# Kernel optimization log

Measured on AMD Instinct MI355X. Metric: run time of the kernel, lower is better.

Reference implementation:

```python
import jax, jax.numpy as jnp
import numpy as np

S, B, D = 2048, 2, 4096
H, KVH, HD = 32, 8, 128          # n_heads_q, n_kv_heads, head_dim
NREP = H // KVH                  # GQA repeat factor
ROPE_BASE = 10000.0


def _rope(x, cos, sin):
    # x: [B, S, h, HD]; cos/sin: [S, HD//2]
    xr = x.reshape(x.shape[:-1] + (-1, 2))
    x0, x1 = xr[..., 0], xr[..., 1]
    c = cos[None, :, None, :]
    s = sin[None, :, None, :]
    out = jnp.stack([x0 * c - x1 * s, x0 * s + x1 * c], axis=-1)
    return out.reshape(x.shape)


def setup_inputs() -> dict:
    key = jax.random.key(0)
    k0, k1, k2, k3, k4 = jax.random.split(key, 5)
    x = jax.random.normal(k0, (S, B, D), jnp.float32)
    inv_freq = 1.0 / (ROPE_BASE ** (np.arange(0, HD, 2, dtype=np.float64) / HD))  # [HD//2]
    t = np.arange(S, dtype=np.float64)[:, None] * inv_freq[None, :]               # [S, HD//2]
    freqs_cos = jnp.asarray(np.cos(t), jnp.float32)
    freqs_sin = jnp.asarray(np.sin(t), jnp.float32)
    scale = 0.02
    wq = jax.random.normal(k1, (H * HD, D), jnp.float32) * scale
    wk = jax.random.normal(k2, (KVH * HD, D), jnp.float32) * scale
    wv = jax.random.normal(k3, (KVH * HD, D), jnp.float32) * scale
    wo = jax.random.normal(k4, (D, H * HD), jnp.float32) * scale
    return {"x": x, "start_pos": 0, "freqs_cos": freqs_cos, "freqs_sin": freqs_sin,
            "wq": wq, "wk": wk, "wv": wv, "wo": wo}


def reference(x, start_pos, freqs_cos, freqs_sin, wq, wk, wv, wo):
    seq_len, batch, _ = x.shape
    # QKV projections (torch Linear: y = x @ W^T), then [S,B,*] -> [B,S,h,HD]
    q = (x @ wq.T).transpose(1, 0, 2).reshape(batch, seq_len, H, HD)
    k = (x @ wk.T).transpose(1, 0, 2).reshape(batch, seq_len, KVH, HD)
    v = (x @ wv.T).transpose(1, 0, 2).reshape(batch, seq_len, KVH, HD)
    # RoPE on q and k
    q = _rope(q, freqs_cos, freqs_sin)
    k = _rope(k, freqs_cos, freqs_sin)
    # repeat_kv (GQA)
    k = jnp.repeat(k, NREP, axis=2)
    v = jnp.repeat(v, NREP, axis=2)
    # [B, H, S, HD]
    q = q.transpose(0, 2, 1, 3)
    k = k.transpose(0, 2, 1, 3)
    v = v.transpose(0, 2, 1, 3)
    # causal scaled dot-product attention (SDPA is_causal=True equivalent)
    scores = jnp.einsum('bhqd,bhkd->bhqk', q, k) / np.float32(np.sqrt(HD))
    causal = jnp.tril(jnp.ones((seq_len, seq_len), dtype=bool))
    scores = jnp.where(causal[None, None], scores, jnp.float32(-jnp.inf))
    probs = jax.nn.softmax(scores.astype(jnp.float32), axis=-1).astype(q.dtype)
    out = jnp.einsum('bhqk,bhkd->bhqd', probs, v)
    # [B,H,S,HD] -> [B,S,H*HD] -> [S,B,H*HD]
    out = out.transpose(0, 2, 1, 3).reshape(batch, seq_len, H * HD).transpose(1, 0, 2)
    return out @ wo.T
```

## Files before the change

### kernel.cpp

```cpp
#include <hip/hip_runtime.h>

typedef __attribute__((ext_vector_type(8))) short s16x8;
typedef __attribute__((ext_vector_type(8))) __bf16 bf16x8;
typedef __attribute__((ext_vector_type(4))) float f32x4;

#define S_LEN 2048
#define KDIM  4096
#define CSOFT 0.12751743f

__device__ __forceinline__ unsigned short f2bf(float f) {
  unsigned u = __builtin_bit_cast(unsigned, f);
  u += 0x7fffu + ((u >> 16) & 1u);
  return (unsigned short)(u >> 16);
}

__device__ __forceinline__ f32x4 mfma_bf16(s16x8 a, s16x8 b, f32x4 c) {
  return __builtin_amdgcn_mfma_f32_16x16x32_bf16(
      __builtin_bit_cast(bf16x8, a), __builtin_bit_cast(bf16x8, b), c, 0, 0, 0);
}

__device__ __forceinline__ void gload_lds16(const unsigned short* g, void* l) {
  __builtin_amdgcn_global_load_lds(
      (const __attribute__((address_space(1))) void*)g,
      (__attribute__((address_space(3))) void*)l, 16, 0, 0);
}

__global__ void cvt_bf16(const float* __restrict__ in,
                         unsigned short* __restrict__ out, int n8) {
  int i = blockIdx.x * 256 + threadIdx.x;
  if (i >= n8) return;
  const float* p = in + (size_t)i * 8;
  f32x4 a = *(const f32x4*)(p);
  f32x4 b = *(const f32x4*)(p + 4);
  s16x8 v;
  v[0] = (short)f2bf(a[0]); v[1] = (short)f2bf(a[1]);
  v[2] = (short)f2bf(a[2]); v[3] = (short)f2bf(a[3]);
  v[4] = (short)f2bf(b[0]); v[5] = (short)f2bf(b[1]);
  v[6] = (short)f2bf(b[2]); v[7] = (short)f2bf(b[3]);
  *(s16x8*)(out + (size_t)i * 8) = v;
}

template <int EPI>
__global__ __launch_bounds__(512, 1)
void gemm256(const unsigned short* __restrict__ A,
             const unsigned short* __restrict__ B,
             void* __restrict__ Out,
             const float* __restrict__ cosT,
             const float* __restrict__ sinT) {
  const int K = KDIM;
  __shared__ __align__(16) unsigned short As[2 * 2 * 8192];
  __shared__ __align__(16) unsigned short Bs[2 * 2 * 8192];

  const int tid = threadIdx.x;
  const int lane = tid & 63, wid = tid >> 6;
  const int l15 = lane & 15, l4 = lane >> 4;
  const int wr = wid >> 2, wc = wid & 3;

  int bid = blockIdx.x;
  int wg = (bid & 7) * 32 + (bid >> 3);
  const int rt = wg >> 4, ct = wg & 15;
  const int row0 = rt * 256, col0 = ct * 256;

  const int ch0 = tid, ch1 = 512 + tid;
  const int sr0 = ch0 >> 3, u0 = (ch0 & 7) ^ (sr0 & 7);
  const int sr1 = ch1 >> 3, u1 = (ch1 & 7) ^ (sr1 & 7);
  const unsigned short* A0p = A + (size_t)(row0 + sr0) * K + u0 * 8;
  const unsigned short* A1p = A + (size_t)(row0 + sr1) * K + u1 * 8;
  const unsigned short* B0p = B + (size_t)(col0 + sr0) * K + u0 * 8;
  const unsigned short* B1p = B + (size_t)(col0 + sr1) * K + u1 * 8;

  const int rdo0 = l15 * 128 + ((l4 ^ (l15 & 7)) << 4);
  const int rdo1 = l15 * 128 + (((4 | l4) ^ (l15 & 7)) << 4);

  f32x4 acc[8][4];
#pragma unroll
  for (int m = 0; m < 8; m++)
#pragma unroll
    for (int n = 0; n < 4; n++) acc[m][n] = f32x4{0.f, 0.f, 0.f, 0.f};

  auto stageA = [&](int buf, int h, int kt) {
    char* d = (char*)As + buf * 32768 + h * 16384 + wid * 1024;
    size_t so = (size_t)h * 128 * K + kt;
    gload_lds16(A0p + so, d);
    gload_lds16(A1p + so, d + 8192);
  };
  auto stageB = [&](int buf, int h, int kt) {
    char* d = (char*)Bs + buf * 32768 + h * 16384 + wid * 1024;
    size_t so = (size_t)h * 128 * K + kt;
    gload_lds16(B0p + so, d);
    gload_lds16(B1p + so, d + 8192);
  };
  auto bar = [&]() {
    __builtin_amdgcn_s_barrier();
    __builtin_amdgcn_sched_barrier(0);
  };
  auto quad = [&](const s16x8* ak0, const s16x8* ak1,
                  const s16x8* bk0, const s16x8* bk1, int mb, int nb) {
    __builtin_amdgcn_s_setprio(1);
#pragma unroll
    for (int mi = 0; mi < 4; mi++)
#pragma unroll
      for (int ni = 0; ni < 2; ni++) {
        acc[mb + mi][nb + ni] =
            mfma_bf16(ak0[mi], bk0[ni], acc[mb + mi][nb + ni]);
        acc[mb + mi][nb + ni] =
            mfma_bf16(ak1[mi], bk1[ni], acc[mb + mi][nb + ni]);
      }
    __builtin_amdgcn_s_setprio(0);
  };

  auto tile4 = [&](int buf, auto st1, auto st2, auto st3, auto st4,
                   int vmEnd) {
    const char* Ab = (const char*)As + buf * 32768 + wr * 16384;
    const char* Bb = (const char*)Bs + buf * 32768 + (wc >> 1) * 16384 +
                     (wc & 1) * 8192;
    s16x8 a0k0[4], a0k1[4], a1k0[4], a1k1[4];
    s16x8 b0k0[2], b0k1[2], b1k0[2], b1k1[2];

#pragma unroll
    for (int mi = 0; mi < 4; mi++) {
      a0k0[mi] = *(const s16x8*)(Ab + mi * 2048 + rdo0);
      a0k1[mi] = *(const s16x8*)(Ab + mi * 2048 + rdo1);
    }
#pragma unroll
    for (int ni = 0; ni < 2; ni++) {
      b0k0[ni] = *(const s16x8*)(Bb + ni * 2048 + rdo0);
      b0k1[ni] = *(const s16x8*)(Bb + ni * 2048 + rdo1);
    }
    st1();
    bar();
    quad(a0k0, a0k1, b0k0, b0k1, 0, 0);
    bar();

#pragma unroll
    for (int mi = 0; mi < 4; mi++) {
      a1k0[mi] = *(const s16x8*)(Ab + 8192 + mi * 2048 + rdo0);
      a1k1[mi] = *(const s16x8*)(Ab + 8192 + mi * 2048 + rdo1);
    }
#pragma unroll
    for (int ni = 0; ni < 2; ni++) {
      b1k0[ni] = *(const s16x8*)(Bb + 4096 + ni * 2048 + rdo0);
      b1k1[ni] = *(const s16x8*)(Bb + 4096 + ni * 2048 + rdo1);
    }
    st2();
    bar();
    quad(a1k0, a1k1, b0k0, b0k1, 4, 0);
    bar();

    st3();
    bar();
    quad(a0k0, a0k1, b1k0, b1k1, 0, 2);
    bar();

    st4();
    bar();
    quad(a1k0, a1k1, b1k0, b1k1, 4, 2);
    if (vmEnd == 4) {
      asm volatile("s_waitcnt vmcnt(4)" ::: "memory");
    } else if (vmEnd == 0) {
      asm volatile("s_waitcnt vmcnt(0)" ::: "memory");
    }
    bar();
  };
  auto nop = [&]() {};

  stageA(0, 0, 0);
  stageA(0, 1, 0);
  stageB(0, 0, 0);
  stageB(0, 1, 0);
  stageA(1, 0, 64);
  stageA(1, 1, 64);
  asm volatile("s_waitcnt vmcnt(4)" ::: "memory");
  bar();

  for (int j = 0; j < 31; j++) {
    const int k1 = (2 * j + 1) * 64, k2 = (2 * j + 2) * 64,
              k3 = (2 * j + 3) * 64;
    tile4(0, [&] { stageB(1, 0, k1); }, [&] { stageB(1, 1, k1); },
          [&] { stageA(0, 0, k2); }, [&] { stageA(0, 1, k2); }, 4);
    tile4(1, [&] { stageB(0, 0, k2); }, [&] { stageB(0, 1, k2); },
          [&] { stageA(1, 0, k3); }, [&] { stageA(1, 1, k3); }, 4);
  }
  {
    const int k1 = 63 * 64;
    tile4(0, [&] { stageB(1, 0, k1); }, [&] { stageB(1, 1, k1); }, nop, nop,
          0);
    tile4(1, nop, nop, nop, nop, -1);
  }

#pragma unroll
  for (int m = 0; m < 8; m++) {
#pragma unroll
    for (int n = 0; n < 4; n++) {
      f32x4 v = acc[m][n];
      int rowb = row0 + wr * 128 + m * 16 + l4 * 4;
      int col = col0 + wc * 64 + n * 16 + l15;
      if (EPI == 3) {
        float* o = (float*)Out;
#pragma unroll
        for (int r = 0; r < 4; r++) o[(size_t)(rowb + r) * 4096 + col] = v[r];
      } else {
        float vp[4];
#pragma unroll
        for (int r = 0; r < 4; r++) vp[r] = __shfl_xor(v[r], 1, 64);
        bool odd = lane & 1;
        int fi = (col & 127) >> 1;
#pragma unroll
        for (int r = 0; r < 4; r++) {
          int nn = rowb + r, s = nn >> 1;
          float c = cosT[s * 64 + fi], sn = sinT[s * 64 + fi];
          v[r] = odd ? (vp[r] * sn + v[r] * c) : (v[r] * c - vp[r] * sn);
        }
        unsigned short* o = (unsigned short*)Out;
        int hh = col >> 7, hd = col & 127;
#pragma unroll
        for (int r = 0; r < 4; r++) {
          int nn = rowb + r, s = nn >> 1, b = nn & 1;
          o[((size_t)(b * 32 + hh) * 2048 + s) * 128 + hd] = f2bf(v[r]);
        }
      }
    }
  }
}

template <int EPI, int N, bool B_FP32>
__global__ __launch_bounds__(256, 2)
void gemm_bt(const unsigned short* __restrict__ A,
             const float* __restrict__ Bw32,
             const unsigned short* __restrict__ Bw16,
             void* __restrict__ Out,
             const float* __restrict__ cosT,
             const float* __restrict__ sinT) {
  const int K = KDIM;
  const int tid = threadIdx.x;
  const int lane = tid & 63, wid = tid >> 6;
  const int l15 = lane & 15, l4 = lane >> 4;
  const int nct = N / 128;
  const int ct = blockIdx.x % nct, rt = blockIdx.x / nct;
  const int row0 = rt * 128, col0 = ct * 128;
  const int wr = wid >> 1, wc = wid & 1;

  __shared__ __align__(16) unsigned short As[128 * 32];
  __shared__ __align__(16) unsigned short Bs[128 * 32];

  f32x4 acc[4][4];
#pragma unroll
  for (int i = 0; i < 4; i++)
#pragma unroll
    for (int j = 0; j < 4; j++) acc[i][j] = f32x4{0.f, 0.f, 0.f, 0.f};

  for (int kt = 0; kt < K; kt += 32) {
#pragma unroll
    for (int i = 0; i < 2; i++) {
      int j = wid * 2 + i;
      int ch = j * 64 + lane;
      int r = ch >> 2, c = ch & 3;
      int sc = c ^ ((r >> 1) & 3);
      gload_lds16(A + (size_t)(row0 + r) * K + kt + sc * 8, (char*)As + j * 1024);
    }
    if (B_FP32) {
#pragma unroll
      for (int j = 0; j < 2; j++) {
        int ch = tid + 256 * j;
        int r = ch >> 2, c = ch & 3;
        const float* src = Bw32 + (size_t)(col0 + r) * K + kt + c * 8;
        f32x4 f0 = *(const f32x4*)(src);
        f32x4 f1 = *(const f32x4*)(src + 4);
        s16x8 v;
        v[0] = (short)f2bf(f0[0]); v[1] = (short)f2bf(f0[1]);
        v[2] = (short)f2bf(f0[2]); v[3] = (short)f2bf(f0[3]);
        v[4] = (short)f2bf(f1[0]); v[5] = (short)f2bf(f1[1]);
        v[6] = (short)f2bf(f1[2]); v[7] = (short)f2bf(f1[3]);
        int sw = c ^ ((r >> 1) & 3);
        *(s16x8*)((char*)Bs + r * 64 + sw * 16) = v;
      }
    } else {
#pragma unroll
      for (int i = 0; i < 2; i++) {
        int j = wid * 2 + i;
        int ch = j * 64 + lane;
        int r = ch >> 2, c = ch & 3;
        int sc = c ^ ((r >> 1) & 3);
        gload_lds16(Bw16 + (size_t)(col0 + r) * K + kt + sc * 8, (char*)Bs + j * 1024);
      }
    }
    __syncthreads();

    s16x8 af[4], bfr[4];
#pragma unroll
    for (int mi = 0; mi < 4; mi++) {
      int r = wr * 64 + mi * 16 + l15;
      int sw = l4 ^ ((r >> 1) & 3);
      af[mi] = *(const s16x8*)((char*)As + r * 64 + sw * 16);
    }
#pragma unroll
    for (int ni = 0; ni < 4; ni++) {
      int r = wc * 64 + ni * 16 + l15;
      int sw = l4 ^ ((r >> 1) & 3);
      bfr[ni] = *(const s16x8*)((char*)Bs + r * 64 + sw * 16);
    }
#pragma unroll
    for (int mi = 0; mi < 4; mi++)
#pragma unroll
      for (int ni = 0; ni < 4; ni++)
        acc[mi][ni] = mfma_bf16(af[mi], bfr[ni], acc[mi][ni]);
    __syncthreads();
  }

#pragma unroll
  for (int mi = 0; mi < 4; mi++) {
#pragma unroll
    for (int ni = 0; ni < 4; ni++) {
      f32x4 v = acc[mi][ni];
      int rowb = row0 + wr * 64 + mi * 16 + l4 * 4;
      int col = col0 + wc * 64 + ni * 16 + l15;
      if (EPI == 3) {
        float* o = (float*)Out;
#pragma unroll
        for (int r = 0; r < 4; r++) o[(size_t)(rowb + r) * 4096 + col] = v[r];
      } else {
        if (EPI != 2) {
          float vp[4];
#pragma unroll
          for (int r = 0; r < 4; r++) vp[r] = __shfl_xor(v[r], 1, 64);
          bool odd = lane & 1;
          int fi = (col & 127) >> 1;
#pragma unroll
          for (int r = 0; r < 4; r++) {
            int n = rowb + r, s = n >> 1;
            float c = cosT[s * 64 + fi], sn = sinT[s * 64 + fi];
            v[r] = odd ? (vp[r] * sn + v[r] * c) : (v[r] * c - vp[r] * sn);
          }
        }
        unsigned short* o = (unsigned short*)Out;
        int hh = col >> 7, hd = col & 127;
#pragma unroll
        for (int r = 0; r < 4; r++) {
          int n = rowb + r, s = n >> 1, b = n & 1;
          size_t idx;
          if (EPI == 0)      idx = ((size_t)(b * 32 + hh) * 2048 + s) * 128 + hd;
          else if (EPI == 1) idx = ((size_t)(b * 8 + hh) * 2048 + s) * 128 + hd;
          else               idx = ((size_t)(b * 8 + hh) * 128 + hd) * 2048 + s;
          o[idx] = f2bf(v[r]);
        }
      }
    }
  }
}

__global__ __launch_bounds__(256, 2)
void attn_fwd(const unsigned short* __restrict__ Qa,
              const unsigned short* __restrict__ Ka,
              const unsigned short* __restrict__ Vt,
              unsigned short* __restrict__ AO) {
  int bid = blockIdx.x;
  int pid = bid & 7;
  int h = (bid >> 3) & 31;
  int b = bid >> 8;
  int kvh = h >> 2;
  int tid = threadIdx.x, lane = tid & 63, wid = tid >> 6;
  int l15 = lane & 15, l4 = lane >> 4;

  __shared__ __align__(16) unsigned short Ks[64 * 128];
  __shared__ __align__(16) unsigned short Vs[128 * 64];
  __shared__ __align__(16) unsigned short Ps[4][32 * 64];

  const unsigned short* Qp = Qa + ((size_t)(b * 32 + h) * 2048) * 128;
  const unsigned short* Kp = Ka + ((size_t)(b * 8 + kvh) * 2048) * 128;
  const unsigned short* Vp = Vt + ((size_t)(b * 8 + kvh) * 128) * 2048;

  for (int half = 0; half < 2; half++) {
    int qt = half == 0 ? (7 - pid) : (8 + pid);
    int q0 = qt * 128, qr0 = q0 + wid * 32;

    s16x8 qf[2][4];
#pragma unroll
    for (int mi = 0; mi < 2; mi++)
#pragma unroll
      for (int ks = 0; ks < 4; ks++)
        qf[mi][ks] = *(const s16x8*)(Qp + (size_t)(qr0 + mi * 16 + l15) * 128 +
                                     ks * 32 + l4 * 8);

    f32x4 o[2][8];
#pragma unroll
    for (int mi = 0; mi < 2; mi++)
#pragma unroll
      for (int nb = 0; nb < 8; nb++) o[mi][nb] = f32x4{0.f, 0.f, 0.f, 0.f};
    float m[2][4], lsum[2][4];
#pragma unroll
    for (int mi = 0; mi < 2; mi++)
#pragma unroll
      for (int pr = 0; pr < 4; pr++) { m[mi][pr] = -1e30f; lsum[mi][pr] = 0.f; }

    int nt = q0 / 64 + 2;
    for (int t = 0; t < nt; t++) {
      int s0 = t * 64;
      const unsigned short* ktp = Kp + (size_t)s0 * 128;
#pragma unroll
      for (int i = 0; i < 4; i++) {
        int j = wid * 4 + i;
        int ch = j * 64 + lane;
        {
          int r = ch >> 4, cl = ch & 15;
          int sc = (cl & 8) | ((cl ^ (r & 7)) & 7);
          gload_lds16(ktp + r * 128 + sc * 8, (char*)Ks + j * 1024);
        }
        {
          int r = ch >> 3, p = ch & 7;
          int sc = p ^ (r & 7);
          gload_lds16(Vp + (size_t)r * 2048 + s0 + sc * 8, (char*)Vs + j * 1024);
        }
      }
      __syncthreads();

      if (s0 <= qr0 + 31) {
        f32x4 sc[2][4];
#pragma unroll
        for (int mi = 0; mi < 2; mi++)
#pragma unroll
          for (int kb = 0; kb < 4; kb++) sc[mi][kb] = f32x4{0.f, 0.f, 0.f, 0.f};
#pragma unroll
        for (int kb = 0; kb < 4; kb++) {
          int r = kb * 16 + l15;
#pragma unroll
          for (int ks = 0; ks < 4; ks++) {
            int c = ks * 4 + l4;
            int sw = (c & 8) | ((c ^ (r & 7)) & 7);
            s16x8 kf = *(const s16x8*)((char*)Ks + r * 256 + sw * 16);
            sc[0][kb] = mfma_bf16(qf[0][ks], kf, sc[0][kb]);
            sc[1][kb] = mfma_bf16(qf[1][ks], kf, sc[1][kb]);
          }
        }
        bool needmask = (s0 + 63) > qr0;
#pragma unroll
        for (int mi = 0; mi < 2; mi++) {
          if (needmask) {
#pragma unroll
            for (int kb = 0; kb < 4; kb++) {
              int kg = s0 + kb * 16 + l15;
#pragma unroll
              for (int pr = 0; pr < 4; pr++) {
                int qg = qr0 + mi * 16 + l4 * 4 + pr;
                if (kg > qg) sc[mi][kb][pr] = -1e30f;
              }
            }
          }
          float rm[4];
#pragma unroll
          for (int pr = 0; pr < 4; pr++)
            rm[pr] = fmaxf(fmaxf(sc[mi][0][pr], sc[mi][1][pr]),
                           fmaxf(sc[mi][2][pr], sc[mi][3][pr]));
#pragma unroll
          for (int xm = 1; xm <= 8; xm <<= 1)
#pragma unroll
            for (int pr = 0; pr < 4; pr++)
              rm[pr] = fmaxf(rm[pr], __shfl_xor(rm[pr], xm, 64));
          bool grow = false;
#pragma unroll
          for (int pr = 0; pr < 4; pr++)
            grow = grow || ((rm[pr] - m[mi][pr]) * CSOFT > 8.f);
          if (__any(grow)) {
            float fac[4];
#pragma unroll
            for (int pr = 0; pr < 4; pr++) {
              float nm = fmaxf(m[mi][pr], rm[pr]);
              fac[pr] = __builtin_amdgcn_exp2f((m[mi][pr] - nm) * CSOFT);
              m[mi][pr] = nm;
              lsum[mi][pr] *= fac[pr];
            }
#pragma unroll
            for (int nb = 0; nb < 8; nb++)
#pragma unroll
              for (int pr = 0; pr < 4; pr++) o[mi][nb][pr] *= fac[pr];
          }
          float rs[4] = {0.f, 0.f, 0.f, 0.f};
#pragma unroll
          for (int kb = 0; kb < 4; kb++)
#pragma unroll
            for (int pr = 0; pr < 4; pr++) {
              float p = __builtin_amdgcn_exp2f((sc[mi][kb][pr] - m[mi][pr]) * CSOFT);
              sc[mi][kb][pr] = p;
              rs[pr] += p;
            }
#pragma unroll
          for (int xm = 1; xm <= 8; xm <<= 1)
#pragma unroll
            for (int pr = 0; pr < 4; pr++) rs[pr] += __shfl_xor(rs[pr], xm, 64);
#pragma unroll
          for (int pr = 0; pr < 4; pr++) lsum[mi][pr] += rs[pr];
          char* pb = (char*)(&Ps[wid][0]);
#pragma unroll
          for (int kb = 0; kb < 4; kb++) {
            int col = kb * 16 + l15;
#pragma unroll
            for (int pr = 0; pr < 4; pr++) {
              int row = mi * 16 + l4 * 4 + pr;
              *(unsigned short*)(pb + row * 128 + (((col >> 3) ^ (row & 7)) * 16) +
                                 (col & 7) * 2) = f2bf(sc[mi][kb][pr]);
            }
          }
        }
        char* pb = (char*)(&Ps[wid][0]);
#pragma unroll
        for (int ks = 0; ks < 2; ks++) {
          s16x8 pa[2];
#pragma unroll
          for (int mi = 0; mi < 2; mi++) {
            int row = mi * 16 + l15;
            int c = ks * 4 + l4;
            pa[mi] = *(const s16x8*)(pb + row * 128 + ((c ^ (row & 7)) * 16));
          }
#pragma unroll
          for (int nb = 0; nb < 8; nb++) {
            int r = nb * 16 + l15;
            int c = ks * 4 + l4;
            s16x8 vf = *(const s16x8*)((char*)Vs + r * 128 + ((c ^ (r & 7)) * 16));
            o[0][nb] = mfma_bf16(pa[0], vf, o[0][nb]);
            o[1][nb] = mfma_bf16(pa[1], vf, o[1][nb]);
          }
        }
      }
      __syncthreads();
    }

#pragma unroll
    for (int mi = 0; mi < 2; mi++) {
      float inv[4];
#pragma unroll
      for (int pr = 0; pr < 4; pr++) inv[pr] = 1.f / lsum[mi][pr];
#pragma unroll
      for (int nb = 0; nb < 8; nb++) {
        int col = h * 128 + nb * 16 + l15;
#pragma unroll
        for (int pr = 0; pr < 4; pr++) {
          int q = qr0 + mi * 16 + l4 * 4 + pr;
          AO[(size_t)(q * 2 + b) * 4096 + col] = f2bf(o[mi][nb][pr] * inv[pr]);
        }
      }
    }
  }
}

extern "C" void kernel_launch(void* const* d_in, const int* in_sizes, int n_in,
                              void* d_out, int out_size, void* d_ws, size_t ws_size,
                              hipStream_t stream) {
  const float* x = (const float*)d_in[0];
  const float* cosT = (const float*)d_in[2];
  const float* sinT = (const float*)d_in[3];
  const float* wq = (const float*)d_in[4];
  const float* wk = (const float*)d_in[5];
  const float* wv = (const float*)d_in[6];
  const float* wo = (const float*)d_in[7];
  float* out = (float*)d_out;

  char* ws = (char*)d_ws;
  unsigned short* xb = (unsigned short*)(ws);
  unsigned short* Qa = (unsigned short*)(ws + 33554432ull);
  unsigned short* Ka = (unsigned short*)(ws + 67108864ull);
  unsigned short* Vt = (unsigned short*)(ws + 75497472ull);
  unsigned short* AO = (unsigned short*)(ws + 83886080ull);
  unsigned short* wqb = (unsigned short*)(ws + 117440512ull);
  unsigned short* wkb = (unsigned short*)(ws + 150994944ull);
  unsigned short* wvb = (unsigned short*)(ws + 159383552ull);
  unsigned short* wob = (unsigned short*)(ws + 167772160ull);
  bool wcvt = ws_size >= 201326592ull;

  cvt_bf16<<<8192, 256, 0, stream>>>(x, xb, 2097152);
  if (wcvt) {
    cvt_bf16<<<8192, 256, 0, stream>>>(wq, wqb, 2097152);
    cvt_bf16<<<2048, 256, 0, stream>>>(wk, wkb, 524288);
    cvt_bf16<<<2048, 256, 0, stream>>>(wv, wvb, 524288);
    cvt_bf16<<<8192, 256, 0, stream>>>(wo, wob, 2097152);
    gemm256<0><<<256, 512, 0, stream>>>(xb, wqb, Qa, cosT, sinT);
    gemm_bt<1, 1024, false><<<256, 256, 0, stream>>>(xb, nullptr, wkb, Ka, cosT, sinT);
    gemm_bt<2, 1024, false><<<256, 256, 0, stream>>>(xb, nullptr, wvb, Vt, cosT, sinT);
  } else {
    gemm_bt<0, 4096, true><<<1024, 256, 0, stream>>>(xb, wq, nullptr, Qa, cosT, sinT);
    gemm_bt<1, 1024, true><<<256, 256, 0, stream>>>(xb, wk, nullptr, Ka, cosT, sinT);
    gemm_bt<2, 1024, true><<<256, 256, 0, stream>>>(xb, wv, nullptr, Vt, cosT, sinT);
  }
  attn_fwd<<<512, 256, 0, stream>>>(Qa, Ka, Vt, AO);
  if (wcvt) {
    gemm256<3><<<256, 512, 0, stream>>>(AO, wob, out, cosT, sinT);
  } else {
    gemm_bt<3, 4096, true><<<1024, 256, 0, stream>>>(AO, wo, nullptr, out, cosT, sinT);
  }
}
```

Measured before the change: 626.4 us.

## Double-buffer K/V tiles in attention and fuse weight conversion launches

After: 645.3 us. +3.0%, slower.

```diff
diff --git a/kernel.cpp b/kernel.cpp
--- a/kernel.cpp
+++ b/kernel.cpp
@@ -25,11 +25,7 @@
       (__attribute__((address_space(3))) void*)l, 16, 0, 0);
 }
 
-__global__ void cvt_bf16(const float* __restrict__ in,
-                         unsigned short* __restrict__ out, int n8) {
-  int i = blockIdx.x * 256 + threadIdx.x;
-  if (i >= n8) return;
-  const float* p = in + (size_t)i * 8;
+__device__ __forceinline__ void cvt8(const float* p, unsigned short* out) {
   f32x4 a = *(const f32x4*)(p);
   f32x4 b = *(const f32x4*)(p + 4);
   s16x8 v;
@@ -37,7 +33,30 @@
   v[2] = (short)f2bf(a[2]); v[3] = (short)f2bf(a[3]);
   v[4] = (short)f2bf(b[0]); v[5] = (short)f2bf(b[1]);
   v[6] = (short)f2bf(b[2]); v[7] = (short)f2bf(b[3]);
-  *(s16x8*)(out + (size_t)i * 8) = v;
+  *(s16x8*)(out) = v;
+}
+
+__global__ void cvt_bf16(const float* __restrict__ in,
+                         unsigned short* __restrict__ out, int n8) {
+  int i = blockIdx.x * 256 + threadIdx.x;
+  if (i >= n8) return;
+  cvt8(in + (size_t)i * 8, out + (size_t)i * 8);
+}
+
+__global__ void cvt_w4(const float* __restrict__ wq, const float* __restrict__ wk,
+                       const float* __restrict__ wv, const float* __restrict__ wo,
+                       unsigned short* __restrict__ oq, unsigned short* __restrict__ ok,
+                       unsigned short* __restrict__ ov, unsigned short* __restrict__ oo) {
+  int blk = blockIdx.x;
+  const float* src;
+  unsigned short* dst;
+  int i;
+  if (blk < 8192) { src = wq; dst = oq; i = blk; }
+  else if (blk < 10240) { src = wk; dst = ok; i = blk - 8192; }
+  else if (blk < 12288) { src = wv; dst = ov; i = blk - 10240; }
+  else { src = wo; dst = oo; i = blk - 12288; }
+  size_t idx = ((size_t)i * 256 + threadIdx.x) * 8;
+  cvt8(src + idx, dst + idx);
 }
 
 template <int EPI>
@@ -90,10 +109,7 @@
     gload_lds16(B0p + so, d);
     gload_lds16(B1p + so, d + 8192);
   };
-  auto bar = [&]() {
-    __builtin_amdgcn_s_barrier();
-    __builtin_amdgcn_sched_barrier(0);
-  };
+  auto bar = [&]() { __builtin_amdgcn_s_barrier(); };
   auto quad = [&](const s16x8* ak0, const s16x8* ak1,
                   const s16x8* bk0, const s16x8* bk1, int mb, int nb) {
     __builtin_amdgcn_s_setprio(1);
@@ -361,14 +377,26 @@
   int tid = threadIdx.x, lane = tid & 63, wid = tid >> 6;
   int l15 = lane & 15, l4 = lane >> 4;
 
-  __shared__ __align__(16) unsigned short Ks[64 * 128];
-  __shared__ __align__(16) unsigned short Vs[128 * 64];
+  __shared__ __align__(16) unsigned short Ks[2][64 * 128];
+  __shared__ __align__(16) unsigned short Vs[2][128 * 64];
   __shared__ __align__(16) unsigned short Ps[4][32 * 64];
 
   const unsigned short* Qp = Qa + ((size_t)(b * 32 + h) * 2048) * 128;
   const unsigned short* Kp = Ka + ((size_t)(b * 8 + kvh) * 2048) * 128;
   const unsigned short* Vp = Vt + ((size_t)(b * 8 + kvh) * 128) * 2048;
 
+  int koff[4], vof[4], dst[4];
+#pragma unroll
+  for (int i = 0; i < 4; i++) {
+    int j = wid * 4 + i;
+    int ch = j * 64 + lane;
+    dst[i] = j * 1024;
+    int kr = ch >> 4, kc = ch & 15;
+    koff[i] = kr * 128 + ((kc & 8) | ((kc ^ (kr & 7)) & 7)) * 8;
+    int vr = ch >> 3, vpp = ch & 7;
+    vof[i] = vr * 2048 + (vpp ^ (vr & 7)) * 8;
+  }
+
   for (int half = 0; half < 2; half++) {
     int qt = half == 0 ? (7 - pid) : (8 + pid);
     int q0 = qt * 128, qr0 = q0 + wid * 32;
@@ -393,32 +421,36 @@
       for (int pr = 0; pr < 4; pr++) { m[mi][pr] = -1e30f; lsum[mi][pr] = 0.f; }
 
     int nt = q0 / 64 + 2;
+
+#pragma unroll
+    for (int i = 0; i < 4; i++) {
+      gload_lds16(Kp + koff[i], (char*)&Ks[0][0] + dst[i]);
+      gload_lds16(Vp + vof[i], (char*)&Vs[0][0] + dst[i]);
+    }
+    asm volatile("s_waitcnt vmcnt(0)" ::: "memory");
+    __builtin_amdgcn_s_barrier();
+
     for (int t = 0; t < nt; t++) {
+      int buf = t & 1;
+      if (t + 1 < nt) {
+        int s1 = (t + 1) * 64;
+        const unsigned short* kb_ = Kp + (size_t)s1 * 128;
+#pragma unroll
+        for (int i = 0; i < 4; i++) {
+          gload_lds16(kb_ + koff[i], (char*)&Ks[buf ^ 1][0] + dst[i]);
+          gload_lds16(Vp + s1 + vof[i], (char*)&Vs[buf ^ 1][0] + dst[i]);
+        }
+      }
       int s0 = t * 64;
-      const unsigned short* ktp = Kp + (size_t)s0 * 128;
-#pragma unroll
-      for (int i = 0; i < 4; i++) {
-        int j = wid * 4 + i;
-        int ch = j * 64 + lane;
-        {
-          int r = ch >> 4, cl = ch & 15;
-          int sc = (cl & 8) | ((cl ^ (r & 7)) & 7);
-          gload_lds16(ktp + r * 128 + sc * 8, (char*)Ks + j * 1024);
-        }
-        {
-          int r = ch >> 3, p = ch & 7;
-          int sc = p ^ (r & 7);
-          gload_lds16(Vp + (size_t)r * 2048 + s0 + sc * 8, (char*)Vs + j * 1024);
-        }
-      }
-      __syncthreads();
-
       if (s0 <= qr0 + 31) {
+        const char* Kb = (const char*)&Ks[buf][0];
+        const char* Vb = (const char*)&Vs[buf][0];
         f32x4 sc[2][4];
 #pragma unroll
         for (int mi = 0; mi < 2; mi++)
 #pragma unroll
           for (int kb = 0; kb < 4; kb++) sc[mi][kb] = f32x4{0.f, 0.f, 0.f, 0.f};
+        __builtin_amdgcn_s_setprio(1);
 #pragma unroll
         for (int kb = 0; kb < 4; kb++) {
           int r = kb * 16 + l15;
@@ -426,11 +458,12 @@
           for (int ks = 0; ks < 4; ks++) {
             int c = ks * 4 + l4;
             int sw = (c & 8) | ((c ^ (r & 7)) & 7);
-            s16x8 kf = *(const s16x8*)((char*)Ks + r * 256 + sw * 16);
+            s16x8 kf = *(const s16x8*)(Kb + r * 256 + sw * 16);
             sc[0][kb] = mfma_bf16(qf[0][ks], kf, sc[0][kb]);
             sc[1][kb] = mfma_bf16(qf[1][ks], kf, sc[1][kb]);
           }
         }
+        __builtin_amdgcn_s_setprio(0);
         bool needmask = (s0 + 63) > qr0;
 #pragma unroll
         for (int mi = 0; mi < 2; mi++) {
@@ -501,6 +534,7 @@
           }
         }
         char* pb = (char*)(&Ps[wid][0]);
+        __builtin_amdgcn_s_setprio(1);
 #pragma unroll
         for (int ks = 0; ks < 2; ks++) {
           s16x8 pa[2];
@@ -514,13 +548,15 @@
           for (int nb = 0; nb < 8; nb++) {
             int r = nb * 16 + l15;
             int c = ks * 4 + l4;
-            s16x8 vf = *(const s16x8*)((char*)Vs + r * 128 + ((c ^ (r & 7)) * 16));
+            s16x8 vf = *(const s16x8*)(Vb + r * 128 + ((c ^ (r & 7)) * 16));
             o[0][nb] = mfma_bf16(pa[0], vf, o[0][nb]);
             o[1][nb] = mfma_bf16(pa[1], vf, o[1][nb]);
           }
         }
-      }
-      __syncthreads();
+        __builtin_amdgcn_s_setprio(0);
+      }
+      asm volatile("s_waitcnt vmcnt(0)" ::: "memory");
+      __builtin_amdgcn_s_barrier();
     }
 
 #pragma unroll
@@ -567,10 +603,7 @@
 
   cvt_bf16<<<8192, 256, 0, stream>>>(x, xb, 2097152);
   if (wcvt) {
-    cvt_bf16<<<8192, 256, 0, stream>>>(wq, wqb, 2097152);
-    cvt_bf16<<<2048, 256, 0, stream>>>(wk, wkb, 524288);
-    cvt_bf16<<<2048, 256, 0, stream>>>(wv, wvb, 524288);
-    cvt_bf16<<<8192, 256, 0, stream>>>(wo, wob, 2097152);
+    cvt_w4<<<20480, 256, 0, stream>>>(wq, wk, wv, wo, wqb, wkb, wvb, wob);
     gemm256<0><<<256, 512, 0, stream>>>(xb, wqb, Qa, cosT, sinT);
     gemm_bt<1, 1024, false><<<256, 256, 0, stream>>>(xb, nullptr, wkb, Ka, cosT, sinT);
     gemm_bt<2, 1024, false><<<256, 256, 0, stream>>>(xb, nullptr, wvb, Vt, cosT, sinT);
```
